# Kernel tuning notes

Hardware: AMD Instinct MI355X
Metric: run time of the kernel (lower is better)

The kernel has to match this reference:

```python
import jax, jax.numpy as jnp
import numpy as np

N_NODES = 50000
N_EDGES = 800000
IN_DIM, HID_DIM, OUT_DIM = 128, 128, 64


def gcn_conv(x, edge_index, W, b):
    """PyG-style GCNConv: out = D^{-1/2}(A+I)D^{-1/2} (x W) + b."""
    n = x.shape[0]
    loops = jnp.arange(n, dtype=edge_index.dtype)
    src = jnp.concatenate([edge_index[0], loops])  # [E+N]
    dst = jnp.concatenate([edge_index[1], loops])
    # symmetric normalization with self-loops
    deg = jax.ops.segment_sum(jnp.ones(dst.shape, x.dtype), dst, num_segments=n)
    dinv = jnp.where(deg > 0, jax.lax.rsqrt(deg), 0.0)
    norm = dinv[src] * dinv[dst]  # [E+N]
    h = x @ W  # transform first (PyG order), [n, d_out]
    msg = h[src] * norm[:, None]  # gather + scale, [E+N, d_out]
    return jax.ops.segment_sum(msg, dst, num_segments=n) + b


def setup_inputs() -> dict:
    key = jax.random.key(0)
    k = jax.random.split(key, 6)
    x = jax.random.normal(k[0], (N_NODES, IN_DIM), jnp.float32)
    edge_index = jax.random.randint(k[1], (2, N_EDGES), 0, N_NODES, dtype=jnp.int32)
    W1 = jax.random.normal(k[2], (IN_DIM, HID_DIM), jnp.float32) * (1.0 / np.sqrt(IN_DIM))
    b1 = jnp.zeros((HID_DIM,), jnp.float32)
    W2 = jax.random.normal(k[3], (HID_DIM, OUT_DIM), jnp.float32) * (1.0 / np.sqrt(HID_DIM))
    b2 = jnp.zeros((OUT_DIM,), jnp.float32)
    return {"x": x, "edge_index": edge_index, "W1": W1, "b1": b1, "W2": W2, "b2": b2}


def reference(x, edge_index, W1, b1, W2, b2):
    h1 = jax.nn.relu(gcn_conv(x, edge_index, W1, b1))
    h2 = gcn_conv(h1, edge_index, W2, b2)
    return (h2, h1)
```

## Files before the change

### kernel.cpp

```cpp
#include <hip/hip_runtime.h>
#include <hip/hip_bf16.h>

constexpr int NN  = 50000;
constexpr int NN2 = 50048;
constexpr int NE  = 800000;
constexpr int SCAN_B = 1024;
constexpr int NB = (NN + SCAN_B - 1) / SCAN_B;
constexpr int GB = (NN + 63) / 64;
constexpr int RANK_BLOCKS = (NE + 255) / 256;
constexpr int RANK4_BLOCKS = (NE / 4 + 255) / 256;

typedef short bf16x8 __attribute__((ext_vector_type(8)));
typedef float f32x4  __attribute__((ext_vector_type(4)));

__device__ __forceinline__ float bfu_to_f(unsigned int u16) {
    return __uint_as_float(u16 << 16);
}
__device__ __forceinline__ unsigned short f_to_bfu(float f) {
    unsigned int u = __float_as_uint(f);
    return (unsigned short)((u + 0x7fffu + ((u >> 16) & 1u)) >> 16);
}
__device__ __forceinline__ void split_bf16(float v, unsigned short& h, unsigned short& l) {
    h = f_to_bfu(v);
    l = f_to_bfu(v - bfu_to_f(h));
}

__device__ __forceinline__ int xcc_id() {
    int x;
    asm volatile("s_getreg_b32 %0, hwreg(HW_REG_XCC_ID, 0, 4)" : "=s"(x));
    return x & 7;
}

__global__ __launch_bounds__(256) void wprep_kernel(
        const float* __restrict__ W1, const float* __restrict__ W2,
        unsigned short* __restrict__ wt1h, unsigned short* __restrict__ wt1l,
        unsigned short* __restrict__ wt2h, unsigned short* __restrict__ wt2l) {
    int i = blockIdx.x * 256 + threadIdx.x;
    if (i < 128 * 128) {
        int n = i >> 7, k = i & 127;
        unsigned short h, l;
        split_bf16(W1[k * 128 + n], h, l);
        wt1h[i] = h; wt1l[i] = l;
    }
    i -= 128 * 128;
    if (i >= 0 && i < 64 * 128) {
        int n = i >> 7, k = i & 127;
        unsigned short h, l;
        split_bf16(W2[k * 64 + n], h, l);
        wt2h[i] = h; wt2l[i] = l;
    }
}

template <int BN, bool RANK>
__global__ __launch_bounds__(256) void mfma_gemm_kernel(
        const float* __restrict__ X,
        const unsigned short* __restrict__ Wth,
        const unsigned short* __restrict__ Wtl,
        unsigned short* __restrict__ H, int M,
        const int* __restrict__ dst, int* __restrict__ cnt, int* __restrict__ pos) {
    __shared__ unsigned short Ah[64 * 128];
    __shared__ unsigned short Al[64 * 128];

    const int bid = blockIdx.x;
    if constexpr (RANK) {
        if (bid >= GB) {
            int e0 = ((bid - GB) * 256 + threadIdx.x) * 4;
            if (e0 < NE) {
                const int rep = xcc_id();
                const int repb = rep << 24;
                int* c = cnt + rep * NN2;
                int4 d = *reinterpret_cast<const int4*>(dst + e0);
                int r0 = __hip_atomic_fetch_add(&c[d.x], 1, __ATOMIC_RELAXED, __HIP_MEMORY_SCOPE_WORKGROUP);
                int r1 = __hip_atomic_fetch_add(&c[d.y], 1, __ATOMIC_RELAXED, __HIP_MEMORY_SCOPE_WORKGROUP);
                int r2 = __hip_atomic_fetch_add(&c[d.z], 1, __ATOMIC_RELAXED, __HIP_MEMORY_SCOPE_WORKGROUP);
                int r3 = __hip_atomic_fetch_add(&c[d.w], 1, __ATOMIC_RELAXED, __HIP_MEMORY_SCOPE_WORKGROUP);
                *reinterpret_cast<int4*>(pos + e0) =
                    make_int4(r0 | repb, r1 | repb, r2 | repb, r3 | repb);
            }
            return;
        }
    }

    const int tid = threadIdx.x;
    const int rb  = bid * 64;

    {
        const float4* Xv = reinterpret_cast<const float4*>(X);
        char* AhB = reinterpret_cast<char*>(Ah);
        char* AlB = reinterpret_cast<char*>(Al);
        for (int i = tid; i < 64 * 32; i += 256) {
            int r = i >> 5, c4 = i & 31;
            float4 v = make_float4(0.f, 0.f, 0.f, 0.f);
            if (rb + r < M) v = Xv[(size_t)(rb + r) * 32 + c4];
            ushort4 hi, lo;
            split_bf16(v.x, hi.x, lo.x);
            split_bf16(v.y, hi.y, lo.y);
            split_bf16(v.z, hi.z, lo.z);
            split_bf16(v.w, hi.w, lo.w);
            int b = (c4 * 8) ^ ((r & 7) << 4);
            *reinterpret_cast<ushort4*>(AhB + r * 256 + b) = hi;
            *reinterpret_cast<ushort4*>(AlB + r * 256 + b) = lo;
        }
    }
    __syncthreads();

    const int lane = tid & 63;
    const int wv   = tid >> 6;
    constexpr int CT = BN / 64;
    const int wc0  = wv * (BN / 4);
    const int lr   = lane & 15;
    const int lg   = lane >> 4;

    f32x4 acc[4][CT];
#pragma unroll
    for (int rt = 0; rt < 4; rt++)
#pragma unroll
        for (int ct = 0; ct < CT; ct++)
            acc[rt][ct] = (f32x4){0.f, 0.f, 0.f, 0.f};

    const char* AhB = reinterpret_cast<const char*>(Ah);
    const char* AlB = reinterpret_cast<const char*>(Al);

#pragma unroll
    for (int k0 = 0; k0 < 128; k0 += 32) {
        bf16x8 ah[4], al[4];
#pragma unroll
        for (int rt = 0; rt < 4; rt++) {
            int row = rt * 16 + lr;
            int inb = (k0 * 2 + lg * 16) ^ ((row & 7) << 4);
            ah[rt] = *reinterpret_cast<const bf16x8*>(AhB + row * 256 + inb);
            al[rt] = *reinterpret_cast<const bf16x8*>(AlB + row * 256 + inb);
        }
#pragma unroll
        for (int ct = 0; ct < CT; ct++) {
            int n = wc0 + ct * 16 + lr;
            int off = n * 128 + k0 + lg * 8;
            bf16x8 bh = *reinterpret_cast<const bf16x8*>(Wth + off);
            bf16x8 bl = *reinterpret_cast<const bf16x8*>(Wtl + off);
#pragma unroll
            for (int rt = 0; rt < 4; rt++) {
                acc[rt][ct] = __builtin_amdgcn_mfma_f32_16x16x32_bf16(ah[rt], bh, acc[rt][ct], 0, 0, 0);
                acc[rt][ct] = __builtin_amdgcn_mfma_f32_16x16x32_bf16(ah[rt], bl, acc[rt][ct], 0, 0, 0);
                acc[rt][ct] = __builtin_amdgcn_mfma_f32_16x16x32_bf16(al[rt], bh, acc[rt][ct], 0, 0, 0);
            }
        }
    }

#pragma unroll
    for (int rt = 0; rt < 4; rt++)
#pragma unroll
        for (int ct = 0; ct < CT; ct++) {
            int col = wc0 + ct * 16 + lr;
#pragma unroll
            for (int j = 0; j < 4; j++) {
                int row = rb + rt * 16 + lg * 4 + j;
                if (row < M) H[(size_t)row * BN + col] = f_to_bfu(acc[rt][ct][j]);
            }
        }
}

__global__ __launch_bounds__(256) void reduce_kernel(const int* __restrict__ cnt,
                                                     int* __restrict__ deg,
                                                     int* __restrict__ roff,
                                                     float* __restrict__ dinv,
                                                     int* __restrict__ bsum, int n) {
    __shared__ int wred[4];
    const int tid = threadIdx.x, lane = tid & 63, wid = tid >> 6;
    int t0 = blockIdx.x * SCAN_B + tid * 4;
    int local = 0;
#pragma unroll
    for (int j = 0; j < 4; j++) {
        int t = t0 + j;
        if (t < n) {
            int acc = 0;
#pragma unroll
            for (int r = 0; r < 8; r++) {
                roff[r * NN2 + t] = acc;
                acc += cnt[r * NN2 + t];
            }
            deg[t] = acc;
            dinv[t] = rsqrtf((float)acc + 1.0f);
            local += acc;
        }
    }
#pragma unroll
    for (int off = 32; off >= 1; off >>= 1) local += __shfl_xor(local, off);
    if (lane == 0) wred[wid] = local;
    __syncthreads();
    if (tid == 0) bsum[blockIdx.x] = wred[0] + wred[1] + wred[2] + wred[3];
}

__global__ __launch_bounds__(64) void scan_tops(const int* __restrict__ bsum,
                                                int* __restrict__ boff,
                                                int* __restrict__ total_out, int nb) {
    int lane = threadIdx.x;
    int v = (lane < nb) ? bsum[lane] : 0;
    int incl = v;
#pragma unroll
    for (int off = 1; off < 64; off <<= 1) {
        int t = __shfl_up(incl, off, 64);
        if (lane >= off) incl += t;
    }
    if (lane < nb) boff[lane] = incl - v;
    if (lane == 63) total_out[0] = incl;
}

__global__ __launch_bounds__(256) void scan_fill(const int* __restrict__ deg,
                                                 const int* __restrict__ boff,
                                                 int* __restrict__ rowptr, int n) {
    __shared__ int wsum[4];
    __shared__ int woff[4];
    const int tid = threadIdx.x, lane = tid & 63, wid = tid >> 6;
    int idx = blockIdx.x * SCAN_B + tid * 4;
    int v0 = (idx + 0 < n) ? deg[idx + 0] : 0;
    int v1 = (idx + 1 < n) ? deg[idx + 1] : 0;
    int v2 = (idx + 2 < n) ? deg[idx + 2] : 0;
    int v3 = (idx + 3 < n) ? deg[idx + 3] : 0;
    int local = v0 + v1 + v2 + v3;
    int incl = local;
#pragma unroll
    for (int off = 1; off < 64; off <<= 1) {
        int t = __shfl_up(incl, off, 64);
        if (lane >= off) incl += t;
    }
    if (lane == 63) wsum[wid] = incl;
    __syncthreads();
    if (tid == 0) {
        int acc = boff[blockIdx.x];
        for (int w = 0; w < 4; w++) { woff[w] = acc; acc += wsum[w]; }
    }
    __syncthreads();
    int p = woff[wid] + (incl - local);
    if (idx + 0 < n) rowptr[idx + 0] = p; p += v0;
    if (idx + 1 < n) rowptr[idx + 1] = p; p += v1;
    if (idx + 2 < n) rowptr[idx + 2] = p; p += v2;
    if (idx + 3 < n) rowptr[idx + 3] = p;
}

__global__ __launch_bounds__(256) void place_kernel(const int* __restrict__ src,
                                                    const int* __restrict__ dst,
                                                    const int* __restrict__ rowptr,
                                                    const int* __restrict__ roff,
                                                    const int* __restrict__ pos,
                                                    unsigned short* __restrict__ srcs,
                                                    int E) {
    int e = blockIdx.x * 256 + threadIdx.x;
    if (e >= E) return;
    int t = dst[e];
    int pr = pos[e];
    int rep = pr >> 24;
    srcs[rowptr[t] + roff[rep * NN2 + t] + (pr & 0xffffff)] = (unsigned short)src[e];
}

template <int NW, bool RELU>
__global__ __launch_bounds__(256) void gather_kernel(const int* __restrict__ rowptr,
                                                     const unsigned short* __restrict__ srcs,
                                                     const float* __restrict__ dinv,
                                                     const unsigned short* __restrict__ h,
                                                     const float* __restrict__ b,
                                                     float* __restrict__ out, int M) {
    constexpr int LPR = NW / 8;
    constexpr int RPW = 64 / LPR;
    const int lane = threadIdx.x & 63;
    const int wid  = threadIdx.x >> 6;
    const int t    = blockIdx.x * 4 + wid;
    if (t >= M) return;
    const int sl = lane % LPR;
    const int sr = lane / LPR;

    float acc[8];
#pragma unroll
    for (int c = 0; c < 8; c++) acc[c] = 0.f;

    const int beg = rowptr[t], end = rowptr[t + 1];
    for (int eb = beg; eb < end; eb += 64) {
        const int rem = end - eb;
        int   sv = 0;
        float wv = 0.f;
        if (lane < rem) { sv = (int)srcs[eb + lane]; wv = dinv[sv]; }
        const int m = rem < 64 ? rem : 64;
        for (int j = 0; j < m; j += RPW) {
            int   s = __shfl(sv, j + sr);
            float w = __shfl(wv, j + sr);
            bf16x8 hv = *reinterpret_cast<const bf16x8*>(h + (size_t)s * NW + sl * 8);
#pragma unroll
            for (int c = 0; c < 8; c++)
                acc[c] += w * bfu_to_f((unsigned short)hv[c]);
        }
    }

#pragma unroll
    for (int off = LPR; off < 64; off <<= 1)
#pragma unroll
        for (int c = 0; c < 8; c++) acc[c] += __shfl_xor(acc[c], off);

    if (sr == 0) {
        const float di = dinv[t];
        bf16x8 own = *reinterpret_cast<const bf16x8*>(h + (size_t)t * NW + sl * 8);
        float4 b0 = *reinterpret_cast<const float4*>(b + sl * 8);
        float4 b1 = *reinterpret_cast<const float4*>(b + sl * 8 + 4);
        float v[8];
#pragma unroll
        for (int c = 0; c < 8; c++) {
            float bc = (c < 4) ? (&b0.x)[c] : (&b1.x)[c - 4];
            v[c] = acc[c] * di + bfu_to_f((unsigned short)own[c]) * di * di + bc;
            if (RELU) v[c] = fmaxf(v[c], 0.f);
        }
        float* op = out + (size_t)t * NW + sl * 8;
        *reinterpret_cast<float4*>(op)     = make_float4(v[0], v[1], v[2], v[3]);
        *reinterpret_cast<float4*>(op + 4) = make_float4(v[4], v[5], v[6], v[7]);
    }
}

extern "C" void kernel_launch(void* const* d_in, const int* in_sizes, int n_in,
                              void* d_out, int out_size, void* d_ws, size_t ws_size,
                              hipStream_t stream) {
    const float* x  = (const float*)d_in[0];
    const int*   ei = (const int*)d_in[1];
    const float* W1 = (const float*)d_in[2];
    const float* b1 = (const float*)d_in[3];
    const float* W2 = (const float*)d_in[4];
    const float* b2 = (const float*)d_in[5];

    float* out_h2 = (float*)d_out;
    float* out_h1 = out_h2 + (size_t)NN * 64;

    const int* src = ei;
    const int* dst = ei + NE;

    int*   wsw    = (int*)d_ws;
    int*   cnt    = wsw;
    int*   deg    = wsw + 400384;
    int*   rowptr = wsw + 450432;
    float* dinv   = (float*)(wsw + 500496);
    int*   bsum   = wsw + 550544;
    int*   boff   = wsw + 550608;
    int*   pos    = wsw + 550672;
    int*   roff   = wsw + 1350672;
    unsigned short* srcs = (unsigned short*)(wsw + 1751056);
    unsigned short* T    = (unsigned short*)(wsw + 2151056);
    unsigned short* wt1h = (unsigned short*)(wsw + 5351056);
    unsigned short* wt1l = (unsigned short*)(wsw + 5359248);
    unsigned short* wt2h = (unsigned short*)(wsw + 5367440);
    unsigned short* wt2l = (unsigned short*)(wsw + 5371536);

    wprep_kernel<<<96, 256, 0, stream>>>(W1, W2, wt1h, wt1l, wt2h, wt2l);
    hipMemsetAsync(cnt, 0, 8 * NN2 * sizeof(int), stream);

    mfma_gemm_kernel<128, true><<<GB + RANK4_BLOCKS, 256, 0, stream>>>(
        x, wt1h, wt1l, T, NN, dst, cnt, pos);

    reduce_kernel<<<NB, 256, 0, stream>>>(cnt, deg, roff, dinv, bsum, NN);
    scan_tops<<<1, 64, 0, stream>>>(bsum, boff, rowptr + NN, NB);
    scan_fill<<<NB, 256, 0, stream>>>(deg, boff, rowptr, NN);
    place_kernel<<<RANK_BLOCKS, 256, 0, stream>>>(src, dst, rowptr, roff, pos, srcs, NE);

    const int aB = (NN + 3) / 4;

    gather_kernel<128, true><<<aB, 256, 0, stream>>>(rowptr, srcs, dinv, T,
                                                     b1, out_h1, NN);
    mfma_gemm_kernel<64, false><<<GB, 256, 0, stream>>>(
        out_h1, wt2h, wt2l, T, NN, nullptr, nullptr, nullptr);
    gather_kernel<64, false><<<aB, 256, 0, stream>>>(rowptr, srcs, dinv, T,
                                                     b2, out_h2, NN);
}
```

Baseline: 226.6 us.

## Replace per-XCC rank counting with single degree histogram and cursor-based placement

The per-XCC replicated counters, stored per-edge ranks and three-kernel reduce/scan pipeline are replaced. A single global degree array is zeroed inside the weight-prep launch, which removes the memset. Degrees are counted with device-scope atomics, and one scan kernel computes each block's prefix by re-summing all earlier degrees. Placement then assigns slots through atomic cursors instead of precomputed ranks. This cuts launches and memory traffic for pos/roff, but adds cross-XCC atomic contention, makes neighbor order nondeterministic, and adds redundant prefix reads in the scan.

```diff
diff --git a/kernel.cpp b/kernel.cpp
--- a/kernel.cpp
+++ b/kernel.cpp
@@ -7,8 +7,7 @@
 constexpr int SCAN_B = 1024;
 constexpr int NB = (NN + SCAN_B - 1) / SCAN_B;
 constexpr int GB = (NN + 63) / 64;
-constexpr int RANK_BLOCKS = (NE + 255) / 256;
-constexpr int RANK4_BLOCKS = (NE / 4 + 255) / 256;
+constexpr int E4_BLOCKS = (NE / 4 + 255) / 256;
 
 typedef short bf16x8 __attribute__((ext_vector_type(8)));
 typedef float f32x4  __attribute__((ext_vector_type(4)));
@@ -25,17 +24,18 @@
     l = f_to_bfu(v - bfu_to_f(h));
 }
 
-__device__ __forceinline__ int xcc_id() {
-    int x;
-    asm volatile("s_getreg_b32 %0, hwreg(HW_REG_XCC_ID, 0, 4)" : "=s"(x));
-    return x & 7;
-}
-
 __global__ __launch_bounds__(256) void wprep_kernel(
         const float* __restrict__ W1, const float* __restrict__ W2,
         unsigned short* __restrict__ wt1h, unsigned short* __restrict__ wt1l,
-        unsigned short* __restrict__ wt2h, unsigned short* __restrict__ wt2l) {
-    int i = blockIdx.x * 256 + threadIdx.x;
+        unsigned short* __restrict__ wt2h, unsigned short* __restrict__ wt2l,
+        int* __restrict__ deg) {
+    const int bid = blockIdx.x;
+    if (bid >= 96) {
+        int i = ((bid - 96) * 256 + threadIdx.x) * 4;
+        if (i < NN2) *reinterpret_cast<int4*>(deg + i) = make_int4(0, 0, 0, 0);
+        return;
+    }
+    int i = bid * 256 + threadIdx.x;
     if (i < 128 * 128) {
         int n = i >> 7, k = i & 127;
         unsigned short h, l;
@@ -51,31 +51,26 @@
     }
 }
 
-template <int BN, bool RANK>
+template <int BN, bool DEG>
 __global__ __launch_bounds__(256) void mfma_gemm_kernel(
         const float* __restrict__ X,
         const unsigned short* __restrict__ Wth,
         const unsigned short* __restrict__ Wtl,
         unsigned short* __restrict__ H, int M,
-        const int* __restrict__ dst, int* __restrict__ cnt, int* __restrict__ pos) {
+        const int* __restrict__ dst, int* __restrict__ deg) {
     __shared__ unsigned short Ah[64 * 128];
     __shared__ unsigned short Al[64 * 128];
 
     const int bid = blockIdx.x;
-    if constexpr (RANK) {
+    if constexpr (DEG) {
         if (bid >= GB) {
             int e0 = ((bid - GB) * 256 + threadIdx.x) * 4;
             if (e0 < NE) {
-                const int rep = xcc_id();
-                const int repb = rep << 24;
-                int* c = cnt + rep * NN2;
                 int4 d = *reinterpret_cast<const int4*>(dst + e0);
-                int r0 = __hip_atomic_fetch_add(&c[d.x], 1, __ATOMIC_RELAXED, __HIP_MEMORY_SCOPE_WORKGROUP);
-                int r1 = __hip_atomic_fetch_add(&c[d.y], 1, __ATOMIC_RELAXED, __HIP_MEMORY_SCOPE_WORKGROUP);
-                int r2 = __hip_atomic_fetch_add(&c[d.z], 1, __ATOMIC_RELAXED, __HIP_MEMORY_SCOPE_WORKGROUP);
-                int r3 = __hip_atomic_fetch_add(&c[d.w], 1, __ATOMIC_RELAXED, __HIP_MEMORY_SCOPE_WORKGROUP);
-                *reinterpret_cast<int4*>(pos + e0) =
-                    make_int4(r0 | repb, r1 | repb, r2 | repb, r3 | repb);
+                atomicAdd(&deg[d.x], 1);
+                atomicAdd(&deg[d.y], 1);
+                atomicAdd(&deg[d.z], 1);
+                atomicAdd(&deg[d.w], 1);
             }
             return;
         }
@@ -159,59 +154,27 @@
         }
 }
 
-__global__ __launch_bounds__(256) void reduce_kernel(const int* __restrict__ cnt,
-                                                     int* __restrict__ deg,
-                                                     int* __restrict__ roff,
-                                                     float* __restrict__ dinv,
-                                                     int* __restrict__ bsum, int n) {
+__global__ __launch_bounds__(256) void scan_kernel(const int* __restrict__ deg,
+                                                   int* __restrict__ rowptr,
+                                                   int* __restrict__ cursor,
+                                                   float* __restrict__ dinv, int n) {
     __shared__ int wred[4];
-    const int tid = threadIdx.x, lane = tid & 63, wid = tid >> 6;
-    int t0 = blockIdx.x * SCAN_B + tid * 4;
-    int local = 0;
-#pragma unroll
-    for (int j = 0; j < 4; j++) {
-        int t = t0 + j;
-        if (t < n) {
-            int acc = 0;
-#pragma unroll
-            for (int r = 0; r < 8; r++) {
-                roff[r * NN2 + t] = acc;
-                acc += cnt[r * NN2 + t];
-            }
-            deg[t] = acc;
-            dinv[t] = rsqrtf((float)acc + 1.0f);
-            local += acc;
-        }
-    }
-#pragma unroll
-    for (int off = 32; off >= 1; off >>= 1) local += __shfl_xor(local, off);
-    if (lane == 0) wred[wid] = local;
-    __syncthreads();
-    if (tid == 0) bsum[blockIdx.x] = wred[0] + wred[1] + wred[2] + wred[3];
-}
-
-__global__ __launch_bounds__(64) void scan_tops(const int* __restrict__ bsum,
-                                                int* __restrict__ boff,
-                                                int* __restrict__ total_out, int nb) {
-    int lane = threadIdx.x;
-    int v = (lane < nb) ? bsum[lane] : 0;
-    int incl = v;
-#pragma unroll
-    for (int off = 1; off < 64; off <<= 1) {
-        int t = __shfl_up(incl, off, 64);
-        if (lane >= off) incl += t;
-    }
-    if (lane < nb) boff[lane] = incl - v;
-    if (lane == 63) total_out[0] = incl;
-}
-
-__global__ __launch_bounds__(256) void scan_fill(const int* __restrict__ deg,
-                                                 const int* __restrict__ boff,
-                                                 int* __restrict__ rowptr, int n) {
     __shared__ int wsum[4];
     __shared__ int woff[4];
     const int tid = threadIdx.x, lane = tid & 63, wid = tid >> 6;
-    int idx = blockIdx.x * SCAN_B + tid * 4;
+    const int b = blockIdx.x;
+
+    const int4* deg4 = reinterpret_cast<const int4*>(deg);
+    int s = 0;
+    for (int i = tid; i < b * 256; i += 256) {
+        int4 v = deg4[i];
+        s += v.x + v.y + v.z + v.w;
+    }
+#pragma unroll
+    for (int off = 32; off >= 1; off >>= 1) s += __shfl_xor(s, off);
+    if (lane == 0) wred[wid] = s;
+
+    int idx = b * SCAN_B + tid * 4;
     int v0 = (idx + 0 < n) ? deg[idx + 0] : 0;
     int v1 = (idx + 1 < n) ? deg[idx + 1] : 0;
     int v2 = (idx + 2 < n) ? deg[idx + 2] : 0;
@@ -226,30 +189,40 @@
     if (lane == 63) wsum[wid] = incl;
     __syncthreads();
     if (tid == 0) {
-        int acc = boff[blockIdx.x];
+        int acc = wred[0] + wred[1] + wred[2] + wred[3];
         for (int w = 0; w < 4; w++) { woff[w] = acc; acc += wsum[w]; }
     }
     __syncthreads();
     int p = woff[wid] + (incl - local);
-    if (idx + 0 < n) rowptr[idx + 0] = p; p += v0;
-    if (idx + 1 < n) rowptr[idx + 1] = p; p += v1;
-    if (idx + 2 < n) rowptr[idx + 2] = p; p += v2;
-    if (idx + 3 < n) rowptr[idx + 3] = p;
-}
-
-__global__ __launch_bounds__(256) void place_kernel(const int* __restrict__ src,
-                                                    const int* __restrict__ dst,
-                                                    const int* __restrict__ rowptr,
-                                                    const int* __restrict__ roff,
-                                                    const int* __restrict__ pos,
-                                                    unsigned short* __restrict__ srcs,
-                                                    int E) {
-    int e = blockIdx.x * 256 + threadIdx.x;
-    if (e >= E) return;
-    int t = dst[e];
-    int pr = pos[e];
-    int rep = pr >> 24;
-    srcs[rowptr[t] + roff[rep * NN2 + t] + (pr & 0xffffff)] = (unsigned short)src[e];
+    int v[4] = {v0, v1, v2, v3};
+#pragma unroll
+    for (int j = 0; j < 4; j++) {
+        int t = idx + j;
+        if (t <= n) rowptr[t] = p;
+        if (t < n) {
+            cursor[t] = p;
+            dinv[t] = rsqrtf((float)v[j] + 1.0f);
+        }
+        p += v[j];
+    }
+}
+
+__global__ __launch_bounds__(256, 8) void place_kernel(const int* __restrict__ src,
+                                                       const int* __restrict__ dst,
+                                                       int* __restrict__ cursor,
+                                                       unsigned short* __restrict__ srcs) {
+    int e0 = (blockIdx.x * 256 + threadIdx.x) * 4;
+    if (e0 >= NE) return;
+    int4 d = *reinterpret_cast<const int4*>(dst + e0);
+    int4 s = *reinterpret_cast<const int4*>(src + e0);
+    int r0 = atomicAdd(&cursor[d.x], 1);
+    int r1 = atomicAdd(&cursor[d.y], 1);
+    int r2 = atomicAdd(&cursor[d.z], 1);
+    int r3 = atomicAdd(&cursor[d.w], 1);
+    srcs[r0] = (unsigned short)s.x;
+    srcs[r1] = (unsigned short)s.y;
+    srcs[r2] = (unsigned short)s.z;
+    srcs[r3] = (unsigned short)s.w;
 }
 
 template <int NW, bool RELU>
@@ -329,38 +302,31 @@
     const int* dst = ei + NE;
 
     int*   wsw    = (int*)d_ws;
-    int*   cnt    = wsw;
-    int*   deg    = wsw + 400384;
-    int*   rowptr = wsw + 450432;
-    float* dinv   = (float*)(wsw + 500496);
-    int*   bsum   = wsw + 550544;
-    int*   boff   = wsw + 550608;
-    int*   pos    = wsw + 550672;
-    int*   roff   = wsw + 1350672;
-    unsigned short* srcs = (unsigned short*)(wsw + 1751056);
-    unsigned short* T    = (unsigned short*)(wsw + 2151056);
-    unsigned short* wt1h = (unsigned short*)(wsw + 5351056);
-    unsigned short* wt1l = (unsigned short*)(wsw + 5359248);
-    unsigned short* wt2h = (unsigned short*)(wsw + 5367440);
-    unsigned short* wt2l = (unsigned short*)(wsw + 5371536);
-
-    wprep_kernel<<<96, 256, 0, stream>>>(W1, W2, wt1h, wt1l, wt2h, wt2l);
-    hipMemsetAsync(cnt, 0, 8 * NN2 * sizeof(int), stream);
-
-    mfma_gemm_kernel<128, true><<<GB + RANK4_BLOCKS, 256, 0, stream>>>(
-        x, wt1h, wt1l, T, NN, dst, cnt, pos);
-
-    reduce_kernel<<<NB, 256, 0, stream>>>(cnt, deg, roff, dinv, bsum, NN);
-    scan_tops<<<1, 64, 0, stream>>>(bsum, boff, rowptr + NN, NB);
-    scan_fill<<<NB, 256, 0, stream>>>(deg, boff, rowptr, NN);
-    place_kernel<<<RANK_BLOCKS, 256, 0, stream>>>(src, dst, rowptr, roff, pos, srcs, NE);
+    int*   deg    = wsw;
+    int*   rowptr = wsw + 50048;
+    int*   cursor = wsw + 100112;
+    float* dinv   = (float*)(wsw + 150160);
+    unsigned short* srcs = (unsigned short*)(wsw + 200208);
+    unsigned short* T    = (unsigned short*)(wsw + 600208);
+    unsigned short* wt1h = (unsigned short*)(wsw + 3800208);
+    unsigned short* wt1l = (unsigned short*)(wsw + 3808400);
+    unsigned short* wt2h = (unsigned short*)(wsw + 3816592);
+    unsigned short* wt2l = (unsigned short*)(wsw + 3820688);
+
+    wprep_kernel<<<145, 256, 0, stream>>>(W1, W2, wt1h, wt1l, wt2h, wt2l, deg);
+
+    mfma_gemm_kernel<128, true><<<GB + E4_BLOCKS, 256, 0, stream>>>(
+        x, wt1h, wt1l, T, NN, dst, deg);
+
+    scan_kernel<<<NB, 256, 0, stream>>>(deg, rowptr, cursor, dinv, NN);
+    place_kernel<<<E4_BLOCKS, 256, 0, stream>>>(src, dst, cursor, srcs);
 
     const int aB = (NN + 3) / 4;
 
     gather_kernel<128, true><<<aB, 256, 0, stream>>>(rowptr, srcs, dinv, T,
                                                      b1, out_h1, NN);
     mfma_gemm_kernel<64, false><<<GB, 256, 0, stream>>>(
-        out_h1, wt2h, wt2l, T, NN, nullptr, nullptr, nullptr);
+        out_h1, wt2h, wt2l, T, NN, nullptr, nullptr);
     gather_kernel<64, false><<<aB, 256, 0, stream>>>(rowptr, srcs, dinv, T,
                                                      b2, out_h2, NN);
 }
```

Measured after the change: 258.9 us. +14.3%, slower.

## Fuse counter zeroing into weight prep and collapse three-kernel scan into one

Applied to the files above, without the earlier changes.

The memset of the per-replica count array moves into extra blocks of the weight-prep kernel. The reduce/scan_tops/scan_fill chain becomes a single scan kernel in which each block recomputes its prefix offset by summing all preceding count entries directly. This removes two kernel launches, a memset, and the deg/bsum/boff intermediates. The cost is redundant reads: later blocks re-read up to the whole 8xNN2 count array, giving quadratic total traffic across 49 blocks, though it is small and likely L2-resident.

```diff
diff --git a/kernel.cpp b/kernel.cpp
--- a/kernel.cpp
+++ b/kernel.cpp
@@ -9,6 +9,7 @@
 constexpr int GB = (NN + 63) / 64;
 constexpr int RANK_BLOCKS = (NE + 255) / 256;
 constexpr int RANK4_BLOCKS = (NE / 4 + 255) / 256;
+constexpr int ZB = (8 * NN2 / 4 + 255) / 256;
 
 typedef short bf16x8 __attribute__((ext_vector_type(8)));
 typedef float f32x4  __attribute__((ext_vector_type(4)));
@@ -34,8 +35,15 @@
 __global__ __launch_bounds__(256) void wprep_kernel(
         const float* __restrict__ W1, const float* __restrict__ W2,
         unsigned short* __restrict__ wt1h, unsigned short* __restrict__ wt1l,
-        unsigned short* __restrict__ wt2h, unsigned short* __restrict__ wt2l) {
-    int i = blockIdx.x * 256 + threadIdx.x;
+        unsigned short* __restrict__ wt2h, unsigned short* __restrict__ wt2l,
+        int* __restrict__ cnt) {
+    const int bid = blockIdx.x;
+    if (bid >= 96) {
+        int i = ((bid - 96) * 256 + threadIdx.x) * 4;
+        if (i < 8 * NN2) *reinterpret_cast<int4*>(cnt + i) = make_int4(0, 0, 0, 0);
+        return;
+    }
+    int i = bid * 256 + threadIdx.x;
     if (i < 128 * 128) {
         int n = i >> 7, k = i & 127;
         unsigned short h, l;
@@ -159,82 +167,66 @@
         }
 }
 
-__global__ __launch_bounds__(256) void reduce_kernel(const int* __restrict__ cnt,
-                                                     int* __restrict__ deg,
-                                                     int* __restrict__ roff,
-                                                     float* __restrict__ dinv,
-                                                     int* __restrict__ bsum, int n) {
+__global__ __launch_bounds__(256) void scan_kernel(const int* __restrict__ cnt,
+                                                   int* __restrict__ roff,
+                                                   int* __restrict__ rowptr,
+                                                   float* __restrict__ dinv, int n) {
     __shared__ int wred[4];
+    __shared__ int wsum[4];
+    __shared__ int woff[4];
     const int tid = threadIdx.x, lane = tid & 63, wid = tid >> 6;
-    int t0 = blockIdx.x * SCAN_B + tid * 4;
-    int local = 0;
+    const int b = blockIdx.x;
+
+    int s = 0;
+#pragma unroll
+    for (int r = 0; r < 8; r++) {
+        const int4* c4 = reinterpret_cast<const int4*>(cnt + r * NN2);
+        for (int i = tid; i < b * 256; i += 256) {
+            int4 v = c4[i];
+            s += v.x + v.y + v.z + v.w;
+        }
+    }
+#pragma unroll
+    for (int off = 32; off >= 1; off >>= 1) s += __shfl_xor(s, off);
+    if (lane == 0) wred[wid] = s;
+
+    int idx = b * SCAN_B + tid * 4;
+    int v[4];
 #pragma unroll
     for (int j = 0; j < 4; j++) {
-        int t = t0 + j;
+        int t = idx + j;
+        int acc = 0;
         if (t < n) {
-            int acc = 0;
 #pragma unroll
             for (int r = 0; r < 8; r++) {
                 roff[r * NN2 + t] = acc;
                 acc += cnt[r * NN2 + t];
             }
-            deg[t] = acc;
             dinv[t] = rsqrtf((float)acc + 1.0f);
-            local += acc;
-        }
-    }
-#pragma unroll
-    for (int off = 32; off >= 1; off >>= 1) local += __shfl_xor(local, off);
-    if (lane == 0) wred[wid] = local;
-    __syncthreads();
-    if (tid == 0) bsum[blockIdx.x] = wred[0] + wred[1] + wred[2] + wred[3];
-}
-
-__global__ __launch_bounds__(64) void scan_tops(const int* __restrict__ bsum,
-                                                int* __restrict__ boff,
-                                                int* __restrict__ total_out, int nb) {
-    int lane = threadIdx.x;
-    int v = (lane < nb) ? bsum[lane] : 0;
-    int incl = v;
+        }
+        v[j] = acc;
+    }
+    int local = v[0] + v[1] + v[2] + v[3];
+    int incl = local;
 #pragma unroll
     for (int off = 1; off < 64; off <<= 1) {
         int t = __shfl_up(incl, off, 64);
         if (lane >= off) incl += t;
     }
-    if (lane < nb) boff[lane] = incl - v;
-    if (lane == 63) total_out[0] = incl;
-}
-
-__global__ __launch_bounds__(256) void scan_fill(const int* __restrict__ deg,
-                                                 const int* __restrict__ boff,
-                                                 int* __restrict__ rowptr, int n) {
-    __shared__ int wsum[4];
-    __shared__ int woff[4];
-    const int tid = threadIdx.x, lane = tid & 63, wid = tid >> 6;
-    int idx = blockIdx.x * SCAN_B + tid * 4;
-    int v0 = (idx + 0 < n) ? deg[idx + 0] : 0;
-    int v1 = (idx + 1 < n) ? deg[idx + 1] : 0;
-    int v2 = (idx + 2 < n) ? deg[idx + 2] : 0;
-    int v3 = (idx + 3 < n) ? deg[idx + 3] : 0;
-    int local = v0 + v1 + v2 + v3;
-    int incl = local;
-#pragma unroll
-    for (int off = 1; off < 64; off <<= 1) {
-        int t = __shfl_up(incl, off, 64);
-        if (lane >= off) incl += t;
-    }
     if (lane == 63) wsum[wid] = incl;
     __syncthreads();
     if (tid == 0) {
-        int acc = boff[blockIdx.x];
+        int acc = wred[0] + wred[1] + wred[2] + wred[3];
         for (int w = 0; w < 4; w++) { woff[w] = acc; acc += wsum[w]; }
     }
     __syncthreads();
     int p = woff[wid] + (incl - local);
-    if (idx + 0 < n) rowptr[idx + 0] = p; p += v0;
-    if (idx + 1 < n) rowptr[idx + 1] = p; p += v1;
-    if (idx + 2 < n) rowptr[idx + 2] = p; p += v2;
-    if (idx + 3 < n) rowptr[idx + 3] = p;
+#pragma unroll
+    for (int j = 0; j < 4; j++) {
+        int t = idx + j;
+        if (t <= n) rowptr[t] = p;
+        p += v[j];
+    }
 }
 
 __global__ __launch_bounds__(256) void place_kernel(const int* __restrict__ src,
@@ -330,29 +322,23 @@
 
     int*   wsw    = (int*)d_ws;
     int*   cnt    = wsw;
-    int*   deg    = wsw + 400384;
-    int*   rowptr = wsw + 450432;
-    float* dinv   = (float*)(wsw + 500496);
-    int*   bsum   = wsw + 550544;
-    int*   boff   = wsw + 550608;
-    int*   pos    = wsw + 550672;
-    int*   roff   = wsw + 1350672;
-    unsigned short* srcs = (unsigned short*)(wsw + 1751056);
-    unsigned short* T    = (unsigned short*)(wsw + 2151056);
-    unsigned short* wt1h = (unsigned short*)(wsw + 5351056);
-    unsigned short* wt1l = (unsigned short*)(wsw + 5359248);
-    unsigned short* wt2h = (unsigned short*)(wsw + 5367440);
-    unsigned short* wt2l = (unsigned short*)(wsw + 5371536);
-
-    wprep_kernel<<<96, 256, 0, stream>>>(W1, W2, wt1h, wt1l, wt2h, wt2l);
-    hipMemsetAsync(cnt, 0, 8 * NN2 * sizeof(int), stream);
+    int*   roff   = wsw + 400384;
+    int*   pos    = wsw + 800768;
+    int*   rowptr = wsw + 1600768;
+    float* dinv   = (float*)(wsw + 1650832);
+    unsigned short* srcs = (unsigned short*)(wsw + 1700880);
+    unsigned short* T    = (unsigned short*)(wsw + 2100880);
+    unsigned short* wt1h = (unsigned short*)(wsw + 5300880);
+    unsigned short* wt1l = (unsigned short*)(wsw + 5309072);
+    unsigned short* wt2h = (unsigned short*)(wsw + 5317264);
+    unsigned short* wt2l = (unsigned short*)(wsw + 5321360);
+
+    wprep_kernel<<<96 + ZB, 256, 0, stream>>>(W1, W2, wt1h, wt1l, wt2h, wt2l, cnt);
 
     mfma_gemm_kernel<128, true><<<GB + RANK4_BLOCKS, 256, 0, stream>>>(
         x, wt1h, wt1l, T, NN, dst, cnt, pos);
 
-    reduce_kernel<<<NB, 256, 0, stream>>>(cnt, deg, roff, dinv, bsum, NN);
-    scan_tops<<<1, 64, 0, stream>>>(bsum, boff, rowptr + NN, NB);
-    scan_fill<<<NB, 256, 0, stream>>>(deg, boff, rowptr, NN);
+    scan_kernel<<<NB, 256, 0, stream>>>(cnt, roff, rowptr, dinv, NN);
     place_kernel<<<RANK_BLOCKS, 256, 0, stream>>>(src, dst, rowptr, roff, pos, srcs, NE);
 
     const int aB = (NN + 3) / 4;
```

After: 256.1 us. 1.13x slower.
